# Kernel tuning notes

Hardware: AMD Instinct MI355X
Metric: run time of the kernel (lower is better)

## Reference

```python
import jax, jax.numpy as jnp
import numpy as np

N = 100000
E = 1600000
IN_DIM = 128
OUT_DIM = 128
NEG_SLOPE = 0.01  # F.leaky_relu default


def setup_inputs() -> dict:
    key = jax.random.key(0)
    k1, k2, k3, k4, k5, k6 = jax.random.split(key, 6)
    feat = jax.random.normal(k1, (N, IN_DIM), dtype=jnp.float32)
    biclique_mask = jax.random.uniform(k2, (IN_DIM,), dtype=jnp.float32)
    W = jax.random.normal(k3, (OUT_DIM, IN_DIM), dtype=jnp.float32) * 0.05
    attn = jax.random.normal(k4, (OUT_DIM,), dtype=jnp.float32) * 0.1
    src = jax.random.randint(k5, (E,), 0, N, dtype=jnp.int32)
    dst = jax.random.randint(k6, (E,), 0, N, dtype=jnp.int32)
    return {"feat": feat, "biclique_mask": biclique_mask, "W": W,
            "attn": attn, "src": src, "dst": dst}


def reference(feat, biclique_mask, W, attn, src, dst):
    # h = Linear(feat * mask), no bias
    h = (feat * biclique_mask[None, :]) @ W.T            # [N, out_dim]
    # edge score depends only on src node -> compute per-node then gather
    s = jax.nn.leaky_relu(h @ attn, negative_slope=NEG_SLOPE)  # [N]
    score = s[src]                                        # [E]
    # edge softmax grouped by destination node
    seg_max = jax.ops.segment_max(score, dst, num_segments=N)  # [N]
    seg_max = jnp.where(jnp.isfinite(seg_max), seg_max, 0.0)   # empty segs
    ex = jnp.exp(score - seg_max[dst])                     # [E]
    denom = jax.ops.segment_sum(ex, dst, num_segments=N)   # [N]
    a = ex / denom[dst]                                    # [E]
    # weighted aggregation: sum_{e: dst(e)=v} h[src(e)] * a[e]
    m = h[src] * a[:, None]                                # [E, out_dim]
    h_new = jax.ops.segment_sum(m, dst, num_segments=N)    # [N, out_dim]
    return jax.nn.relu(h_new)
```

## Files before the change

kernel.cpp:

```cpp
#include <hip/hip_runtime.h>
#include <math.h>

#define NN 100000
#define EE 1600000
#define DIM 128

#define BK 256
#define NBK2 392
#define NCH 256
#define EPB 6250
#define SCN (NBK2 * NCH)
#define NSB 98

#define GEMM_BLKS 1563

#define SRC_MASK 0x1FFFFu

typedef _Float16 half8 __attribute__((ext_vector_type(8)));
typedef float f32x4 __attribute__((ext_vector_type(4)));

__global__ __launch_bounds__(256) void k_wt(const float* __restrict__ W,
                                            const float* __restrict__ mask,
                                            _Float16* __restrict__ Bt) {
    int o = blockIdx.x * 256 + threadIdx.x;
    if (o < DIM * DIM) Bt[o] = (_Float16)(W[o] * mask[o & 127]);
}

__global__ __launch_bounds__(256) void k_front(const float* __restrict__ feat,
                                               const _Float16* __restrict__ Bt,
                                               const float* __restrict__ attn,
                                               _Float16* __restrict__ hh,
                                               _Float16* __restrict__ sv16,
                                               const int* __restrict__ dst,
                                               int* __restrict__ gHist) {
    __shared__ int hist[NBK2];
    const int bx = blockIdx.x;
    const int t  = threadIdx.x;

    if (bx >= GEMM_BLKS) {
        const int b = bx - GEMM_BLKS;
        for (int i = t; i < NBK2; i += 256) hist[i] = 0;
        __syncthreads();
        const int e0 = b * EPB;
        int e1 = e0 + EPB; if (e1 > EE) e1 = EE;
        for (int e = e0 + t; e < e1; e += 256)
            atomicAdd(&hist[dst[e] >> 8], 1);
        __syncthreads();
        for (int i = t; i < NBK2; i += 256)
            gHist[i * NCH + b] = hist[i];
        return;
    }

    const int lane = t & 63;
    const int wv   = t >> 6;
    const int l15  = lane & 15;
    const int quad = lane >> 4;
    const int row0 = bx * 64 + wv * 16;

    f32x4 acc[8];
#pragma unroll
    for (int nt = 0; nt < 8; ++nt) acc[nt] = (f32x4){0.f, 0.f, 0.f, 0.f};

    const int arow = row0 + l15;
    const bool okA = arow < NN;
    const float* ap = feat + (size_t)(okA ? arow : 0) * DIM + quad * 8;

#pragma unroll
    for (int kc = 0; kc < 4; ++kc) {
        half8 a;
        float4 f0 = ((const float4*)(ap + kc * 32))[0];
        float4 f1 = ((const float4*)(ap + kc * 32))[1];
        if (!okA) { f0 = make_float4(0, 0, 0, 0); f1 = make_float4(0, 0, 0, 0); }
        a[0] = (_Float16)f0.x; a[1] = (_Float16)f0.y;
        a[2] = (_Float16)f0.z; a[3] = (_Float16)f0.w;
        a[4] = (_Float16)f1.x; a[5] = (_Float16)f1.y;
        a[6] = (_Float16)f1.z; a[7] = (_Float16)f1.w;
#pragma unroll
        for (int nt = 0; nt < 8; ++nt) {
            half8 b = *(const half8*)(Bt + (size_t)(nt * 16 + l15) * DIM + kc * 32 + quad * 8);
            acc[nt] = __builtin_amdgcn_mfma_f32_16x16x32_f16(a, b, acc[nt], 0, 0, 0);
        }
    }

    float avv[8];
#pragma unroll
    for (int nt = 0; nt < 8; ++nt) avv[nt] = attn[nt * 16 + l15];

#pragma unroll
    for (int r = 0; r < 4; ++r) {
        int row = row0 + quad * 4 + r;
        float p = 0.f;
#pragma unroll
        for (int nt = 0; nt < 8; ++nt) p += acc[nt][r] * avv[nt];
        p += __shfl_xor(p, 1, 64);
        p += __shfl_xor(p, 2, 64);
        p += __shfl_xor(p, 4, 64);
        p += __shfl_xor(p, 8, 64);
        if (l15 == 0 && row < NN) {
            float lr = (p > 0.f) ? p : 0.01f * p;
            sv16[row] = (_Float16)__expf(lr);
        }
    }

#pragma unroll
    for (int nt = 0; nt < 8; ++nt) {
#pragma unroll
        for (int r = 0; r < 4; ++r) {
            int row = row0 + quad * 4 + r;
            if (row < NN)
                hh[(size_t)row * DIM + nt * 16 + l15] = (_Float16)acc[nt][r];
        }
    }
}

__global__ __launch_bounds__(256) void k_scan_a(const int* __restrict__ deg,
                                                int* __restrict__ excl,
                                                int* __restrict__ bsum) {
    __shared__ int wsum[4];
    __shared__ int woff[4];
    const int t = threadIdx.x, b = blockIdx.x;
    const int base = b * 1024 + t * 4;
    int v0 = deg[base + 0];
    int v1 = deg[base + 1];
    int v2 = deg[base + 2];
    int v3 = deg[base + 3];
    int tsum = v0 + v1 + v2 + v3;

    const int lane = t & 63, w = t >> 6;
    int incl = tsum;
#pragma unroll
    for (int d = 1; d < 64; d <<= 1) {
        int n = __shfl_up(incl, d, 64);
        if (lane >= d) incl += n;
    }
    if (lane == 63) wsum[w] = incl;
    __syncthreads();
    if (t == 0) {
        int run = 0;
#pragma unroll
        for (int i = 0; i < 4; ++i) { woff[i] = run; run += wsum[i]; }
        bsum[b] = run;
    }
    __syncthreads();
    int texcl = incl - tsum + woff[w];
    excl[base + 0] = texcl;
    excl[base + 1] = texcl + v0;
    excl[base + 2] = texcl + v0 + v1;
    excl[base + 3] = texcl + v0 + v1 + v2;
}

#define INLINE_BOFF_SCAN(bsum, sboff, swtop, t)                          \
    {                                                                    \
        const int lane_ = (t) & 63;                                      \
        int v_ = 0, incl_ = 0;                                           \
        if ((t) < 128) {                                                 \
            v_ = ((t) < NSB) ? (bsum)[(t)] : 0;                          \
            incl_ = v_;                                                  \
            _Pragma("unroll")                                            \
            for (int d_ = 1; d_ < 64; d_ <<= 1) {                        \
                int n_ = __shfl_up(incl_, d_, 64);                       \
                if (lane_ >= d_) incl_ += n_;                            \
            }                                                            \
            if ((t) == 63) (swtop) = incl_;                              \
        }                                                                \
        __syncthreads();                                                 \
        if ((t) < NSB) {                                                 \
            int add_ = ((t) >= 64) ? (swtop) : 0;                        \
            (sboff)[(t)] = incl_ - v_ + add_;                            \
        }                                                                \
        __syncthreads();                                                 \
    }

__global__ __launch_bounds__(1024) void k_bscatter(const int* __restrict__ src,
                                                   const int* __restrict__ dst,
                                                   const int* __restrict__ gOff,
                                                   const int* __restrict__ bsum,
                                                   unsigned* __restrict__ binned) {
    __shared__ int cur[NBK2];
    __shared__ int sboff[NSB];
    __shared__ int swtop;
    const int t = threadIdx.x, b = blockIdx.x;

    INLINE_BOFF_SCAN(bsum, sboff, swtop, t)

    for (int i = t; i < NBK2; i += 1024) {
        int idx = i * NCH + b;
        cur[i] = gOff[idx] + sboff[idx >> 10];
    }
    __syncthreads();
    const int e0 = b * EPB;
    int e1 = e0 + EPB; if (e1 > EE) e1 = EE;
    for (int e = e0 + t; e < e1; e += 1024) {
        int d  = dst[e];
        int si = src[e];
        int bk   = d >> 8;
        int dloc = d & (BK - 1);
        int pos = atomicAdd(&cur[bk], 1);
        binned[pos] = (unsigned)si | ((unsigned)dloc << 17);
    }
}

__global__ __launch_bounds__(1024) void k_group(const int* __restrict__ gOff,
                                                const int* __restrict__ bsum,
                                                const unsigned* __restrict__ binned,
                                                const _Float16* __restrict__ sv16,
                                                unsigned* __restrict__ pack,
                                                int* __restrict__ offs) {
    __shared__ int ldeg[BK];
    __shared__ int wpart[4];
    __shared__ int sboff[NSB];
    __shared__ int swtop;
    const int bk = blockIdx.x;
    const int t  = threadIdx.x;

    INLINE_BOFF_SCAN(bsum, sboff, swtop, t)

    const int i0 = bk * NCH;
    const int base = gOff[i0] + sboff[i0 >> 10];
    int endp;
    if (bk == NBK2 - 1) endp = EE;
    else {
        int i1 = (bk + 1) * NCH;
        endp = gOff[i1] + sboff[i1 >> 10];
    }

    if (t < BK) ldeg[t] = 0;
    __syncthreads();
    for (int j = base + t; j < endp; j += 1024)
        atomicAdd(&ldeg[(binned[j] >> 17) & (BK - 1)], 1);
    __syncthreads();

    int v = 0, incl = 0;
    const int lane = t & 63;
    if (t < BK) {
        v = ldeg[t];
        incl = v;
#pragma unroll
        for (int d = 1; d < 64; d <<= 1) {
            int n = __shfl_up(incl, d, 64);
            if (lane >= d) incl += n;
        }
        if (lane == 63) wpart[t >> 6] = incl;
    }
    __syncthreads();
    if (t == 0) {
        int run = 0;
#pragma unroll
        for (int i = 0; i < 4; ++i) { int tmp = wpart[i]; wpart[i] = run; run += tmp; }
    }
    __syncthreads();
    if (t < BK) {
        int excl = incl - v + wpart[t >> 6];
        int c = base + excl;
        int n = bk * BK + t;
        if (n < NN) offs[n] = c;
        ldeg[t] = c;
    }
    if (bk == NBK2 - 1 && t == 0) offs[NN] = EE;
    __syncthreads();

    for (int j = base + t; j < endp; j += 1024) {
        unsigned e = binned[j];
        int dloc = (e >> 17) & (BK - 1);
        int si   = e & SRC_MASK;
        unsigned short wb =
            __builtin_bit_cast(unsigned short, sv16[si]);
        int pos = atomicAdd(&ldeg[dloc], 1);
        pack[pos] = (unsigned)si | ((unsigned)wb << 17);
    }
}

__global__ __launch_bounds__(256) void k_agg(const _Float16* __restrict__ hh,
                                             const int* __restrict__ offs,
                                             const unsigned* __restrict__ pack,
                                             float* __restrict__ out) {
    const int lane = threadIdx.x & 63;
    const int g    = lane >> 4;
    const int li   = lane & 15;
    const int wid  = __builtin_amdgcn_readfirstlane(blockIdx.x * 4 + (threadIdx.x >> 6));
    if (wid >= NN) return;
    const int beg = __builtin_amdgcn_readfirstlane(offs[wid]);
    const int end = __builtin_amdgcn_readfirstlane(offs[wid + 1]);
    const int deg = end - beg;

    const half8* h8 = (const half8*)hh;
    float acc[8];
#pragma unroll
    for (int k = 0; k < 8; ++k) acc[k] = 0.f;
    float lsum = 0.f;

    for (int base = 0; base < deg; base += 64) {
        const int nrem = deg - base;
        const int idx  = base + lane;
        const int cl   = (idx < deg) ? idx : (deg - 1);
        const unsigned eraw = pack[beg + cl];
        const unsigned enc = (idx < deg) ? eraw : (eraw & SRC_MASK);
        lsum += (float)__builtin_bit_cast(_Float16,
                                          (unsigned short)(enc >> 17));
        const int cmax = (nrem < 64) ? nrem : 64;
        for (int c0 = 0; c0 < cmax; c0 += 16) {
#pragma unroll
            for (int s = 0; s < 4; ++s) {
                const int ei = c0 + s * 4 + g;
                const unsigned eb =
                    (unsigned)__shfl((int)enc, ei, 64);
                const int   si = eb & SRC_MASK;
                const float wg = (float)__builtin_bit_cast(
                    _Float16, (unsigned short)(eb >> 17));
                half8 v = h8[((unsigned)si << 4) + li];
#pragma unroll
                for (int k = 0; k < 8; ++k)
                    acc[k] = fmaf((float)v[k], wg, acc[k]);
            }
        }
    }

#pragma unroll
    for (int k = 0; k < 8; ++k) {
        acc[k] += __shfl_xor(acc[k], 16, 64);
        acc[k] += __shfl_xor(acc[k], 32, 64);
    }
    lsum += __shfl_xor(lsum, 1, 64);
    lsum += __shfl_xor(lsum, 2, 64);
    lsum += __shfl_xor(lsum, 4, 64);
    lsum += __shfl_xor(lsum, 8, 64);
    lsum += __shfl_xor(lsum, 16, 64);
    lsum += __shfl_xor(lsum, 32, 64);

    const float inv = (lsum > 0.f) ? (1.0f / lsum) : 0.f;

    if (g == 0) {
        float4 o0, o1;
        o0.x = fmaxf(acc[0] * inv, 0.f);
        o0.y = fmaxf(acc[1] * inv, 0.f);
        o0.z = fmaxf(acc[2] * inv, 0.f);
        o0.w = fmaxf(acc[3] * inv, 0.f);
        o1.x = fmaxf(acc[4] * inv, 0.f);
        o1.y = fmaxf(acc[5] * inv, 0.f);
        o1.z = fmaxf(acc[6] * inv, 0.f);
        o1.w = fmaxf(acc[7] * inv, 0.f);
        float4* op = (float4*)(out + (size_t)wid * DIM + li * 8);
        op[0] = o0;
        op[1] = o1;
    }
}

extern "C" void kernel_launch(void* const* d_in, const int* in_sizes, int n_in,
                              void* d_out, int out_size, void* d_ws, size_t ws_size,
                              hipStream_t stream) {
    const float* feat = (const float*)d_in[0];
    const float* mask = (const float*)d_in[1];
    const float* W    = (const float*)d_in[2];
    const float* attn = (const float*)d_in[3];
    const int*   src  = (const int*)d_in[4];
    const int*   dst  = (const int*)d_in[5];
    float* out = (float*)d_out;

    char* ws = (char*)d_ws;
    size_t off = 0;
    auto alloc = [&](size_t bytes) -> void* {
        void* p = ws + off;
        off = (off + bytes + 511) & ~(size_t)511;
        return p;
    };
    _Float16* hh   = (_Float16*)alloc((size_t)NN * DIM * 2);
    _Float16* sv16 = (_Float16*)alloc((size_t)NN * 2);
    _Float16* Bt   = (_Float16*)alloc((size_t)DIM * DIM * 2);
    int*     gOff  = (int*)alloc((size_t)SCN * 4);
    int*     offs  = (int*)alloc((size_t)(NN + 1) * 4);
    int*     bsum  = (int*)alloc((size_t)NSB * 4);
    unsigned* binned = (unsigned*)alloc((size_t)EE * 4);
    unsigned* pack   = (unsigned*)alloc((size_t)EE * 4);

    k_wt<<<(DIM * DIM + 255) / 256, 256, 0, stream>>>(W, mask, Bt);
    k_front<<<GEMM_BLKS + NCH, 256, 0, stream>>>(feat, Bt, attn, hh, sv16,
                                                 dst, gOff);
    k_scan_a<<<NSB, 256, 0, stream>>>(gOff, gOff, bsum);
    k_bscatter<<<NCH, 1024, 0, stream>>>(src, dst, gOff, bsum, binned);
    k_group<<<NBK2, 1024, 0, stream>>>(gOff, bsum, binned, sv16, pack, offs);
    k_agg<<<(NN + 3) / 4, 256, 0, stream>>>(hh, offs, pack, out);
}
```

Before: 230.7 us.

## Quantize node features to int8 with per-row scales for aggregation gathers

Stores the projected features as int8 with a per-row absmax scale instead of fp16, and folds the scale into the per-edge fp16 weight packed during grouping. The softmax denominator is now accumulated per destination in the grouping kernel via shared-memory atomics rather than inside the aggregation kernel. The aim is to halve the bytes gathered per edge in the memory-bound aggregation. It trades accuracy (8-bit quantization error) and adds extra atomics and scale loads in the grouping step.

Measured after the change: 222.2 us. -3.7%, faster.

```diff
diff --git a/kernel.cpp b/kernel.cpp
--- a/kernel.cpp
+++ b/kernel.cpp
@@ -17,6 +17,7 @@
 #define SRC_MASK 0x1FFFFu
 
 typedef _Float16 half8 __attribute__((ext_vector_type(8)));
+typedef signed char char8 __attribute__((ext_vector_type(8)));
 typedef float f32x4 __attribute__((ext_vector_type(4)));
 
 __global__ __launch_bounds__(256) void k_wt(const float* __restrict__ W,
@@ -29,7 +30,8 @@
 __global__ __launch_bounds__(256) void k_front(const float* __restrict__ feat,
                                                const _Float16* __restrict__ Bt,
                                                const float* __restrict__ attn,
-                                               _Float16* __restrict__ hh,
+                                               signed char* __restrict__ hq,
+                                               float* __restrict__ scf,
                                                _Float16* __restrict__ sv16,
                                                const int* __restrict__ dst,
                                                int* __restrict__ gHist) {
@@ -89,26 +91,33 @@
 #pragma unroll
     for (int r = 0; r < 4; ++r) {
         int row = row0 + quad * 4 + r;
-        float p = 0.f;
-#pragma unroll
-        for (int nt = 0; nt < 8; ++nt) p += acc[nt][r] * avv[nt];
+        float p = 0.f, m = 0.f;
+#pragma unroll
+        for (int nt = 0; nt < 8; ++nt) {
+            p += acc[nt][r] * avv[nt];
+            m = fmaxf(m, fabsf(acc[nt][r]));
+        }
         p += __shfl_xor(p, 1, 64);
         p += __shfl_xor(p, 2, 64);
         p += __shfl_xor(p, 4, 64);
         p += __shfl_xor(p, 8, 64);
+        m = fmaxf(m, __shfl_xor(m, 1, 64));
+        m = fmaxf(m, __shfl_xor(m, 2, 64));
+        m = fmaxf(m, __shfl_xor(m, 4, 64));
+        m = fmaxf(m, __shfl_xor(m, 8, 64));
         if (l15 == 0 && row < NN) {
             float lr = (p > 0.f) ? p : 0.01f * p;
             sv16[row] = (_Float16)__expf(lr);
-        }
-    }
-
-#pragma unroll
-    for (int nt = 0; nt < 8; ++nt) {
-#pragma unroll
-        for (int r = 0; r < 4; ++r) {
-            int row = row0 + quad * 4 + r;
-            if (row < NN)
-                hh[(size_t)row * DIM + nt * 16 + l15] = (_Float16)acc[nt][r];
+            scf[row]  = m * (1.f / 127.f);
+        }
+        const float inv_s = (m > 0.f) ? (127.f / m) : 0.f;
+        if (row < NN) {
+#pragma unroll
+            for (int nt = 0; nt < 8; ++nt) {
+                float qv = rintf(acc[nt][r] * inv_s);
+                qv = fminf(fmaxf(qv, -127.f), 127.f);
+                hq[(size_t)row * DIM + nt * 16 + l15] = (signed char)(int)qv;
+            }
         }
     }
 }
@@ -204,9 +213,12 @@
                                                 const int* __restrict__ bsum,
                                                 const unsigned* __restrict__ binned,
                                                 const _Float16* __restrict__ sv16,
+                                                const float* __restrict__ scf,
                                                 unsigned* __restrict__ pack,
-                                                int* __restrict__ offs) {
+                                                int* __restrict__ offs,
+                                                float* __restrict__ lsum) {
     __shared__ int ldeg[BK];
+    __shared__ float lsumSh[BK];
     __shared__ int wpart[4];
     __shared__ int sboff[NSB];
     __shared__ int swtop;
@@ -224,7 +236,7 @@
         endp = gOff[i1] + sboff[i1 >> 10];
     }
 
-    if (t < BK) ldeg[t] = 0;
+    if (t < BK) { ldeg[t] = 0; lsumSh[t] = 0.f; }
     __syncthreads();
     for (int j = base + t; j < endp; j += 1024)
         atomicAdd(&ldeg[(binned[j] >> 17) & (BK - 1)], 1);
@@ -263,16 +275,25 @@
         unsigned e = binned[j];
         int dloc = (e >> 17) & (BK - 1);
         int si   = e & SRC_MASK;
+        float w  = (float)sv16[si];
+        float sc = scf[si];
         unsigned short wb =
-            __builtin_bit_cast(unsigned short, sv16[si]);
+            __builtin_bit_cast(unsigned short, (_Float16)(w * sc));
+        atomicAdd(&lsumSh[dloc], w);
         int pos = atomicAdd(&ldeg[dloc], 1);
         pack[pos] = (unsigned)si | ((unsigned)wb << 17);
     }
-}
-
-__global__ __launch_bounds__(256) void k_agg(const _Float16* __restrict__ hh,
+    __syncthreads();
+    if (t < BK) {
+        int n = bk * BK + t;
+        if (n < NN) lsum[n] = lsumSh[t];
+    }
+}
+
+__global__ __launch_bounds__(256) void k_agg(const signed char* __restrict__ hq,
                                              const int* __restrict__ offs,
                                              const unsigned* __restrict__ pack,
+                                             const float* __restrict__ lsum,
                                              float* __restrict__ out) {
     const int lane = threadIdx.x & 63;
     const int g    = lane >> 4;
@@ -283,11 +304,9 @@
     const int end = __builtin_amdgcn_readfirstlane(offs[wid + 1]);
     const int deg = end - beg;
 
-    const half8* h8 = (const half8*)hh;
     float acc[8];
 #pragma unroll
     for (int k = 0; k < 8; ++k) acc[k] = 0.f;
-    float lsum = 0.f;
 
     for (int base = 0; base < deg; base += 64) {
         const int nrem = deg - base;
@@ -295,8 +314,6 @@
         const int cl   = (idx < deg) ? idx : (deg - 1);
         const unsigned eraw = pack[beg + cl];
         const unsigned enc = (idx < deg) ? eraw : (eraw & SRC_MASK);
-        lsum += (float)__builtin_bit_cast(_Float16,
-                                          (unsigned short)(enc >> 17));
         const int cmax = (nrem < 64) ? nrem : 64;
         for (int c0 = 0; c0 < cmax; c0 += 16) {
 #pragma unroll
@@ -307,10 +324,10 @@
                 const int   si = eb & SRC_MASK;
                 const float wg = (float)__builtin_bit_cast(
                     _Float16, (unsigned short)(eb >> 17));
-                half8 v = h8[((unsigned)si << 4) + li];
+                char8 q = *(const char8*)(hq + ((size_t)(unsigned)si << 7) + li * 8);
 #pragma unroll
                 for (int k = 0; k < 8; ++k)
-                    acc[k] = fmaf((float)v[k], wg, acc[k]);
+                    acc[k] = fmaf((float)q[k], wg, acc[k]);
             }
         }
     }
@@ -320,14 +337,9 @@
         acc[k] += __shfl_xor(acc[k], 16, 64);
         acc[k] += __shfl_xor(acc[k], 32, 64);
     }
-    lsum += __shfl_xor(lsum, 1, 64);
-    lsum += __shfl_xor(lsum, 2, 64);
-    lsum += __shfl_xor(lsum, 4, 64);
-    lsum += __shfl_xor(lsum, 8, 64);
-    lsum += __shfl_xor(lsum, 16, 64);
-    lsum += __shfl_xor(lsum, 32, 64);
-
-    const float inv = (lsum > 0.f) ? (1.0f / lsum) : 0.f;
+
+    const float l   = lsum[wid];
+    const float inv = (l > 0.f) ? (1.0f / l) : 0.f;
 
     if (g == 0) {
         float4 o0, o1;
@@ -363,7 +375,9 @@
         off = (off + bytes + 511) & ~(size_t)511;
         return p;
     };
-    _Float16* hh   = (_Float16*)alloc((size_t)NN * DIM * 2);
+    signed char* hq  = (signed char*)alloc((size_t)NN * DIM);
+    float*   scf  = (float*)alloc((size_t)NN * 4);
+    float*   lsum = (float*)alloc((size_t)NN * 4);
     _Float16* sv16 = (_Float16*)alloc((size_t)NN * 2);
     _Float16* Bt   = (_Float16*)alloc((size_t)DIM * DIM * 2);
     int*     gOff  = (int*)alloc((size_t)SCN * 4);
@@ -373,10 +387,11 @@
     unsigned* pack   = (unsigned*)alloc((size_t)EE * 4);
 
     k_wt<<<(DIM * DIM + 255) / 256, 256, 0, stream>>>(W, mask, Bt);
-    k_front<<<GEMM_BLKS + NCH, 256, 0, stream>>>(feat, Bt, attn, hh, sv16,
-                                                 dst, gOff);
+    k_front<<<GEMM_BLKS + NCH, 256, 0, stream>>>(feat, Bt, attn, hq, scf,
+                                                 sv16, dst, gOff);
     k_scan_a<<<NSB, 256, 0, stream>>>(gOff, gOff, bsum);
     k_bscatter<<<NCH, 1024, 0, stream>>>(src, dst, gOff, bsum, binned);
-    k_group<<<NBK2, 1024, 0, stream>>>(gOff, bsum, binned, sv16, pack, offs);
-    k_agg<<<(NN + 3) / 4, 256, 0, stream>>>(hh, offs, pack, out);
-}
+    k_group<<<NBK2, 1024, 0, stream>>>(gOff, bsum, binned, sv16, scf,
+                                       pack, offs, lsum);
+    k_agg<<<(NN + 3) / 4, 256, 0, stream>>>(hq, offs, pack, lsum, out);
+}
```
